# Kernel tuning notes

Hardware: AMD Instinct MI355X
Metric: run time of the kernel (lower is better)

The kernel has to match this reference:

```python
import jax, jax.numpy as jnp
import numpy as np


def setup_inputs() -> dict:
    key = jax.random.key(0)
    ks = jax.random.split(key, 8)
    B, N, C = 8, 4096, 128
    x = jax.random.normal(ks[0], (B, N, C), dtype=jnp.float32)
    spatial_pos = jax.random.randint(ks[1], (1, N, N), 0, 6, dtype=jnp.int32)
    sc = 1.0 / np.sqrt(C)
    W1 = jax.random.normal(ks[2], (C, C), dtype=jnp.float32) * sc
    b1 = jax.random.normal(ks[3], (C,), dtype=jnp.float32) * 0.01
    W2 = jax.random.normal(ks[4], (C, C // 8), dtype=jnp.float32) * sc
    b2 = jax.random.normal(ks[5], (C // 8,), dtype=jnp.float32) * 0.01
    Wb = jax.random.normal(ks[6], (C + C // 8, C), dtype=jnp.float32) * (1.0 / np.sqrt(C + C // 8))
    bb = jax.random.normal(ks[7], (C,), dtype=jnp.float32) * 0.01
    return {"x": x, "spatial_pos": spatial_pos, "W1": W1, "b1": b1,
            "W2": W2, "b2": b2, "Wb": Wb, "bb": bb}


def reference(x, spatial_pos, W1, b1, W2, b2, Wb, bb):
    # s=1, l=2: scale k=1 uses mask (spatial_pos <= 1), k=2 uses (spatial_pos == 2)
    sp = spatial_pos[0]                      # [N, N], batch-invariant
    m1 = (sp <= 1).astype(x.dtype)           # [N, N]
    m2 = (sp == 2).astype(x.dtype)           # [N, N]
    h1 = x @ W1 + b1                         # [B, N, C]
    h2 = x @ W2 + b2                         # [B, N, C//8]
    # torch.bmm(mask.expand(B,-1,-1), h) == einsum over shared mask
    f1 = jnp.einsum('ij,bjc->bic', m1, h1)   # [B, N, C]
    f2 = jnp.einsum('ij,bjc->bic', m2, h2)   # [B, N, C//8]
    feats = jnp.concatenate([f1, f2], axis=-1)  # [B, N, C + C//8]
    return feats @ Wb + bb                   # [B, N, output_dim]
```

## Files before the change

kernel.cpp:

```cpp
#include <hip/hip_runtime.h>
#include <stdint.h>

typedef unsigned short u16;
typedef __attribute__((ext_vector_type(8))) short short8;
typedef __attribute__((ext_vector_type(4))) float f32x4;
typedef __attribute__((ext_vector_type(16))) float f32x16;

#define MFMA __builtin_amdgcn_mfma_f32_16x16x32_bf16
#define MFMA32 __builtin_amdgcn_mfma_f32_32x32x16_bf16

__device__ __forceinline__ u16 f2bf(float f) {
  union { float f; uint32_t u; } v; v.f = f;
  return (u16)((v.u + 0x7FFFu + ((v.u >> 16) & 1u)) >> 16);
}

#define GLOAD16(gp, lp) \
  __builtin_amdgcn_global_load_lds((const __attribute__((address_space(1))) uint32_t*)(gp), \
                                   (__attribute__((address_space(3))) uint32_t*)(lp), 16, 0, 0)

#define WS_H    0
#define WS_Q1   9502720
#define WS_Q2   9503232
#define WS_M1P  9503744
#define WS_M2P  11600896
#define WS_RS1  13698048
#define WS_RS2  13714432
#define WS_WSB  13730816

__global__ __launch_bounds__(256) void k0(const int* __restrict__ sp,
                                          unsigned long long* __restrict__ m1p,
                                          unsigned long long* __restrict__ m2p,
                                          float* __restrict__ rs1, float* __restrict__ rs2,
                                          const float* __restrict__ W1, const float* __restrict__ Wb,
                                          const float* __restrict__ b1, const float* __restrict__ b2,
                                          const float* __restrict__ W2,
                                          float* __restrict__ q1, float* __restrict__ q2,
                                          u16* __restrict__ wsbg) {
  const int tid = threadIdx.x;
  if (blockIdx.x < 1024) {
    int wave = tid >> 6, lane = tid & 63;
    int i = blockIdx.x * 4 + wave;
    const int* rowp = sp + (size_t)i * 4096;
    int c1 = 0, c2 = 0;
    for (int w = 0; w < 64; ++w) {
      int v = rowp[w * 64 + lane];
      unsigned long long bb1 = __ballot(v <= 1);
      unsigned long long bb2 = __ballot(v == 2);
      if (lane == 0) {
        m1p[(size_t)w * 4096 + i] = bb1;
        m2p[(size_t)w * 4096 + i] = bb2;
        c1 += __popcll(bb1);
        c2 += __popcll(bb2);
      }
    }
    if (lane == 0) { rs1[i] = (float)c1; rs2[i] = (float)c2; }
    return;
  }
  int idx = (int)(blockIdx.x - 1024) * 256 + tid;
  int a = idx >> 7, c = idx & 127;
  float acc = 0.f;
  for (int k = 0; k < 128; ++k) acc += W1[a * 128 + k] * Wb[k * 128 + c];
  wsbg[(((a >> 3) * 144) + c) * 8 + (a & 7)] = f2bf(acc);
  if (idx < 2048) {
    int k = idx >> 4, nn2 = idx & 15;
    wsbg[(((k >> 3) * 144) + 128 + nn2) * 8 + (k & 7)] = f2bf(W2[k * 16 + nn2]);
  }
  if (idx < 128) {
    float s1 = 0.f, s2 = 0.f;
    for (int k = 0; k < 128; ++k) s1 += b1[k] * Wb[k * 128 + idx];
    for (int k = 0; k < 16; ++k)  s2 += b2[k] * Wb[(128 + k) * 128 + idx];
    q1[idx] = s1; q2[idx] = s2;
  }
}

__global__ __launch_bounds__(256, 2) void kproj(const float* __restrict__ x,
                                                const u16* __restrict__ wsbg,
                                                u16* __restrict__ H) {
  __shared__ u16 wsb[18432];
  __shared__ u16 xs[64 * 136];
  __shared__ u16 hs[64 * 146];
  const int tid = threadIdx.x;
  const int bid = blockIdx.x;
  const int b = bid >> 6;
  const int kt = bid & 63;
  const size_t r0 = (size_t)b * 4096 + (size_t)kt * 64;

#pragma unroll
  for (int i = 0; i < 9; ++i)
    GLOAD16(wsbg + (i * 256 + tid) * 8, (char*)&wsb[0] + (i * 256 + tid) * 16);
  {
    const float* xp = x + (r0 + (tid >> 2)) * 128 + (tid & 3) * 32;
    u16* xd = xs + (tid >> 2) * 136 + (tid & 3) * 32;
#pragma unroll
    for (int i = 0; i < 4; ++i) {
      f32x4 a = ((const f32x4*)xp)[i * 2];
      f32x4 bq = ((const f32x4*)xp)[i * 2 + 1];
      short8 pk;
      pk[0] = (short)f2bf(a[0]); pk[1] = (short)f2bf(a[1]);
      pk[2] = (short)f2bf(a[2]); pk[3] = (short)f2bf(a[3]);
      pk[4] = (short)f2bf(bq[0]); pk[5] = (short)f2bf(bq[1]);
      pk[6] = (short)f2bf(bq[2]); pk[7] = (short)f2bf(bq[3]);
      *(short8*)(xd + i * 8) = pk;
    }
  }
  __syncthreads();

  const int w = tid >> 6, l = tid & 63, lr = l & 15, lg = l >> 4;
  f32x4 acc[9];
  f32x4 zz = {0.f, 0.f, 0.f, 0.f};
#pragma unroll
  for (int fn = 0; fn < 9; ++fn) acc[fn] = zz;
#pragma unroll
  for (int kf = 0; kf < 4; ++kf) {
    short8 af = *(const short8*)(xs + (w * 16 + lr) * 136 + kf * 32 + lg * 8);
#pragma unroll
    for (int fn = 0; fn < 9; ++fn) {
      short8 bf = *(const short8*)(wsb + (((kf * 4 + lg) * 144) + fn * 16 + lr) * 8);
      acc[fn] = MFMA(af, bf, acc[fn], 0, 0, 0);
    }
  }
  __syncthreads();
#pragma unroll
  for (int fn = 0; fn < 9; ++fn)
#pragma unroll
    for (int g = 0; g < 4; ++g)
      hs[(w * 16 + lg * 4 + g) * 146 + fn * 16 + lr] = f2bf(acc[fn][g]);
  __syncthreads();
  const size_t base = (size_t)kt * 73728 + (size_t)b * 9216;
  for (int i = 0; i < 5; ++i) {
    int ch = i * 256 + tid;
    if (ch < 1152) {
      union { u16 s[8]; uint4 v; } pk;
      size_t di;
      if (ch < 1024) {
        int cb = ch >> 8, ks = (ch >> 6) & 3, ll = ch & 63;
        int row = ks * 16 + (ll >> 5) * 8;
        int col = cb * 32 + (ll & 31);
#pragma unroll
        for (int e = 0; e < 8; ++e) pk.s[e] = hs[(row + e) * 146 + col];
        di = base + (size_t)((cb * 4 + ks) * 512 + ll * 8);
      } else {
        int c2 = ch - 1024;
        int kf = c2 >> 6, ll = c2 & 63;
        int row = kf * 32 + (ll >> 4) * 8;
        int col = 128 + (ll & 15);
#pragma unroll
        for (int e = 0; e < 8; ++e) pk.s[e] = hs[(row + e) * 146 + col];
        di = base + (size_t)(8192 + kf * 512 + ll * 8);
      }
      *(uint4*)(H + di) = pk.v;
    }
  }
}

__device__ __forceinline__ short8 expand_byte(uint32_t wd, int sh) {
  uint32_t b = (wd >> sh) & 0xFFu;
  uint32_t t = b * 0x8001u;
  union { uint32_t u[4]; short8 s; } r;
  r.u[0] = (t & 0x00010001u) * 0x3F80u;
  r.u[1] = (t & 0x00040004u) * 0x0FE0u;
  r.u[2] = (t & 0x00100010u) * 0x03F8u;
  r.u[3] = (t & 0x00400040u) * 0x00FEu;
  return r.s;
}

__global__ __launch_bounds__(512, 2) void kb1(const u16* __restrict__ H,
                                              const char* __restrict__ M1b,
                                              const char* __restrict__ M2b,
                                              const float* __restrict__ rs1, const float* __restrict__ rs2,
                                              const float* __restrict__ q1, const float* __restrict__ q2,
                                              const float* __restrict__ Wb, const float* __restrict__ bb,
                                              float* __restrict__ out) {
  __shared__ u16 bt[3][9216];
  __shared__ u16 mkb[3][1024];
  __shared__ float f2pf[2][128][16];
  __shared__ u16 f2s[128 * 40];
  __shared__ u16 wb2s[2048];

  const int tid = threadIdx.x;
  const int bid = blockIdx.x;
  const int b = bid & 7;
  const int i0 = (bid >> 3) * 128;

  const int w = tid >> 6, l = tid & 63, lr = l & 15, lg = l >> 4;
  const int h2 = w >> 2, cb = w & 3;
  const int rg0 = h2 * 2, rg1 = h2 * 2 + 1;
  const int kfm = h2;
  const int rt0 = cb * 2, rt1 = cb * 2 + 1;
  const int sh32 = (l >> 5) * 8;
  const int lgsh = lg * 8;

  const u16* pB0 = H + (size_t)b * 9216 + (size_t)tid * 8;
  const u16* pB1 = H + (size_t)b * 9216 + (size_t)(512 + tid) * 8;
  const u16* pB2 = H + (size_t)b * 9216 + (size_t)(1024 + tid) * 8;
  const int mc = tid - 128;
  const char* pM = ((mc & 64) ? M2b : M1b) + (size_t)i0 * 8 + (size_t)(mc & 63) * 16;
  const int dB0 = tid * 16, dB1 = (512 + tid) * 16, dB2 = (1024 + tid) * 16;
  const int dM = ((mc >> 6) & 1) * 1024 + (mc & 63) * 16;

#define STAGE(BUF) { \
    GLOAD16(pB0, (char*)&bt[BUF][0] + dB0); \
    GLOAD16(pB1, (char*)&bt[BUF][0] + dB1); \
    if (tid < 128) GLOAD16(pB2, (char*)&bt[BUF][0] + dB2); \
    else if (tid < 256) GLOAD16(pM, (char*)&mkb[BUF][0] + dM); \
    pB0 += 73728; pB1 += 73728; pB2 += 73728; pM += 32768; }

  const int fb0 = (cb * 4) * 512 + l * 8;
  const int fm0 = 8192 + kfm * 512 + l * 8;

  f32x16 am0, am1;
  f32x4 acc2a, acc2b;
#pragma unroll
  for (int i = 0; i < 16; ++i) { am0[i] = 0.f; am1[i] = 0.f; }
  acc2a[0] = acc2a[1] = acc2a[2] = acc2a[3] = 0.f;
  acc2b[0] = acc2b[1] = acc2b[2] = acc2b[3] = 0.f;

#define WAITV { if (w < 4) asm volatile("s_waitcnt vmcnt(3)" ::: "memory"); \
                else asm volatile("s_waitcnt vmcnt(2)" ::: "memory"); }

#define COMPUTE(BUF) { \
    const u16* src_ = &bt[BUF][0]; \
    const char* mk_ = (const char*)&mkb[BUF][0]; \
    uint2 cA_ = *(const uint2*)(mk_ + (rg0 * 32 + (l & 31)) * 8); \
    uint2 cB_ = *(const uint2*)(mk_ + (rg1 * 32 + (l & 31)) * 8); \
    uint32_t cm0_ = *(const uint32_t*)(mk_ + 1024 + (rt0 * 16 + lr) * 8 + kfm * 4); \
    uint32_t cm1_ = *(const uint32_t*)(mk_ + 1024 + (rt1 * 16 + lr) * 8 + kfm * 4); \
    short8 bf0_ = *(const short8*)(src_ + fb0); \
    short8 bf1_ = *(const short8*)(src_ + fb0 + 512); \
    short8 bf2_ = *(const short8*)(src_ + fb0 + 1024); \
    short8 bf3_ = *(const short8*)(src_ + fb0 + 1536); \
    short8 bm_  = *(const short8*)(src_ + fm0); \
    short8 eA0_ = expand_byte(cA_.x, sh32); \
    short8 eA1_ = expand_byte(cA_.x, sh32 + 16); \
    short8 eA2_ = expand_byte(cA_.y, sh32); \
    short8 eA3_ = expand_byte(cA_.y, sh32 + 16); \
    short8 eB0_ = expand_byte(cB_.x, sh32); \
    short8 eB1_ = expand_byte(cB_.x, sh32 + 16); \
    short8 eB2_ = expand_byte(cB_.y, sh32); \
    short8 eB3_ = expand_byte(cB_.y, sh32 + 16); \
    short8 em0_ = expand_byte(cm0_, lgsh); \
    short8 em1_ = expand_byte(cm1_, lgsh); \
    __builtin_amdgcn_s_setprio(1); \
    am0 = MFMA32(eA0_, bf0_, am0, 0, 0, 0); \
    am1 = MFMA32(eB0_, bf0_, am1, 0, 0, 0); \
    am0 = MFMA32(eA1_, bf1_, am0, 0, 0, 0); \
    am1 = MFMA32(eB1_, bf1_, am1, 0, 0, 0); \
    am0 = MFMA32(eA2_, bf2_, am0, 0, 0, 0); \
    am1 = MFMA32(eB2_, bf2_, am1, 0, 0, 0); \
    am0 = MFMA32(eA3_, bf3_, am0, 0, 0, 0); \
    am1 = MFMA32(eB3_, bf3_, am1, 0, 0, 0); \
    acc2a = MFMA(em0_, bm_, acc2a, 0, 0, 0); \
    acc2b = MFMA(em1_, bm_, acc2b, 0, 0, 0); \
    __builtin_amdgcn_s_setprio(0); }

#define PHASE(BUF, BUF2) { WAITV; __builtin_amdgcn_s_barrier(); STAGE(BUF2); COMPUTE(BUF) }

  STAGE(0);
  STAGE(1);

#pragma unroll
  for (int i = 0; i < 4; ++i) {
    int e = i * 512 + tid;
    int cbw = e >> 9, rem = e & 511, ll = rem >> 3, ee = rem & 7;
    wb2s[e] = f2bf(Wb[(128 + (ll >> 5) * 8 + ee) * 128 + cbw * 32 + (ll & 31)]);
  }

  for (int it = 0; it < 20; ++it) {
    PHASE(0, 2);
    PHASE(1, 0);
    PHASE(2, 1);
  }
  PHASE(0, 2);
  PHASE(1, 0);
  { WAITV; __builtin_amdgcn_s_barrier(); COMPUTE(2) }
  { asm volatile("s_waitcnt vmcnt(0)" ::: "memory");
    __builtin_amdgcn_s_barrier(); COMPUTE(0) }

#pragma unroll
  for (int gg = 0; gg < 4; ++gg) {
    f2pf[kfm][rt0 * 16 + lg * 4 + gg][lr] = acc2a[gg];
    f2pf[kfm][rt1 * 16 + lg * 4 + gg][lr] = acc2b[gg];
  }
  __syncthreads();
#pragma unroll
  for (int j = 0; j < 4; ++j) {
    int e = j * 512 + tid;
    int row = e >> 4, col = e & 15;
    f2s[row * 40 + col] = f2bf(f2pf[0][row][col] + f2pf[1][row][col]);
  }
  __syncthreads();

  {
    short8 bw_ = *(const short8*)(wb2s + cb * 512 + l * 8);
    short8 afA = *(const short8*)(f2s + (rg0 * 32 + (l & 31)) * 40 + sh32);
    short8 afB = *(const short8*)(f2s + (rg1 * 32 + (l & 31)) * 40 + sh32);
    am0 = MFMA32(afA, bw_, am0, 0, 0, 0);
    am1 = MFMA32(afB, bw_, am1, 0, 0, 0);
  }

  const int colA = cb * 32 + (l & 31);
  const float q1v = q1[colA], q2v = q2[colA], bbv = bb[colA];
#pragma unroll
  for (int r = 0; r < 16; ++r) {
    int rr = (r & 3) + 8 * (r >> 2) + 4 * (l >> 5);
    {
      int row = rg0 * 32 + rr;
      float r1 = rs1[i0 + row], r2 = rs2[i0 + row];
      out[((size_t)b * 4096 + i0 + row) * 128 + colA] = am0[r] + r1 * q1v + r2 * q2v + bbv;
    }
    {
      int row = rg1 * 32 + rr;
      float r1 = rs1[i0 + row], r2 = rs2[i0 + row];
      out[((size_t)b * 4096 + i0 + row) * 128 + colA] = am1[r] + r1 * q1v + r2 * q2v + bbv;
    }
  }
}

extern "C" void kernel_launch(void* const* d_in, const int* in_sizes, int n_in,
                              void* d_out, int out_size, void* d_ws, size_t ws_size,
                              hipStream_t stream) {
  const float* x  = (const float*)d_in[0];
  const int*   sp = (const int*)d_in[1];
  const float* W1 = (const float*)d_in[2];
  const float* b1 = (const float*)d_in[3];
  const float* W2 = (const float*)d_in[4];
  const float* b2 = (const float*)d_in[5];
  const float* Wb = (const float*)d_in[6];
  const float* bb = (const float*)d_in[7];
  float* out = (float*)d_out;
  char* ws = (char*)d_ws;

  u16* H = (u16*)(ws + WS_H);
  float* q1 = (float*)(ws + WS_Q1);
  float* q2 = (float*)(ws + WS_Q2);
  unsigned long long* m1p = (unsigned long long*)(ws + WS_M1P);
  unsigned long long* m2p = (unsigned long long*)(ws + WS_M2P);
  float* rs1 = (float*)(ws + WS_RS1);
  float* rs2 = (float*)(ws + WS_RS2);
  u16* wsbg = (u16*)(ws + WS_WSB);

  k0<<<1088, 256, 0, stream>>>(sp, m1p, m2p, rs1, rs2, W1, Wb, b1, b2, W2, q1, q2, wsbg);
  kproj<<<512, 256, 0, stream>>>(x, wsbg, H);
  kb1<<<256, 512, 0, stream>>>(H, (const char*)m1p, (const char*)m2p,
                               rs1, rs2, q1, q2, Wb, bb, out);
}
```

Before: 97.00 us.

## Halve kb1 row tile to 64 rows and double grid to 512 blocks

The main mask-aggregation kernel now processes 64 output rows per block instead of 128, and the grid doubles to 512 blocks. Each wave keeps one 32x32 accumulator and one 16x16 accumulator instead of two of each, and the mask staging and wait counts are adjusted to match. The aim is more blocks across the CUs and fewer registers per wave for better occupancy. The cost is that every block still streams the full H matrix for its batch, so reads of H from global or L2 roughly double, and each loaded tile feeds half as many MFMAs.

```diff
diff --git a/kernel.cpp b/kernel.cpp
--- a/kernel.cpp
+++ b/kernel.cpp
@@ -173,20 +173,18 @@
                                               float* __restrict__ out) {
   __shared__ u16 bt[3][9216];
   __shared__ u16 mkb[3][1024];
-  __shared__ float f2pf[2][128][16];
-  __shared__ u16 f2s[128 * 40];
+  __shared__ float f2pf[2][64][16];
+  __shared__ u16 f2s[64 * 40];
   __shared__ u16 wb2s[2048];
 
   const int tid = threadIdx.x;
   const int bid = blockIdx.x;
   const int b = bid & 7;
-  const int i0 = (bid >> 3) * 128;
+  const int i0 = (bid >> 3) * 64;
 
   const int w = tid >> 6, l = tid & 63, lr = l & 15, lg = l >> 4;
-  const int h2 = w >> 2, cb = w & 3;
-  const int rg0 = h2 * 2, rg1 = h2 * 2 + 1;
-  const int kfm = h2;
-  const int rt0 = cb * 2, rt1 = cb * 2 + 1;
+  const int rg = w >> 2, cb = w & 3;
+  const int rt = w & 3, kfm = w >> 2;
   const int sh32 = (l >> 5) * 8;
   const int lgsh = lg * 8;
 
@@ -194,63 +192,50 @@
   const u16* pB1 = H + (size_t)b * 9216 + (size_t)(512 + tid) * 8;
   const u16* pB2 = H + (size_t)b * 9216 + (size_t)(1024 + tid) * 8;
   const int mc = tid - 128;
-  const char* pM = ((mc & 64) ? M2b : M1b) + (size_t)i0 * 8 + (size_t)(mc & 63) * 16;
+  const char* pM = ((mc < 32) ? M1b : M2b) + (size_t)i0 * 8 + (size_t)(mc & 31) * 16;
   const int dB0 = tid * 16, dB1 = (512 + tid) * 16, dB2 = (1024 + tid) * 16;
-  const int dM = ((mc >> 6) & 1) * 1024 + (mc & 63) * 16;
+  const int dM = mc * 16;
 
 #define STAGE(BUF) { \
     GLOAD16(pB0, (char*)&bt[BUF][0] + dB0); \
     GLOAD16(pB1, (char*)&bt[BUF][0] + dB1); \
     if (tid < 128) GLOAD16(pB2, (char*)&bt[BUF][0] + dB2); \
-    else if (tid < 256) GLOAD16(pM, (char*)&mkb[BUF][0] + dM); \
+    else if (tid < 192) GLOAD16(pM, (char*)&mkb[BUF][0] + dM); \
     pB0 += 73728; pB1 += 73728; pB2 += 73728; pM += 32768; }
 
   const int fb0 = (cb * 4) * 512 + l * 8;
   const int fm0 = 8192 + kfm * 512 + l * 8;
 
-  f32x16 am0, am1;
-  f32x4 acc2a, acc2b;
-#pragma unroll
-  for (int i = 0; i < 16; ++i) { am0[i] = 0.f; am1[i] = 0.f; }
-  acc2a[0] = acc2a[1] = acc2a[2] = acc2a[3] = 0.f;
-  acc2b[0] = acc2b[1] = acc2b[2] = acc2b[3] = 0.f;
-
-#define WAITV { if (w < 4) asm volatile("s_waitcnt vmcnt(3)" ::: "memory"); \
+  f32x16 am;
+  f32x4 acc2;
+#pragma unroll
+  for (int i = 0; i < 16; ++i) am[i] = 0.f;
+  acc2[0] = acc2[1] = acc2[2] = acc2[3] = 0.f;
+
+#define WAITV { if (w < 3) asm volatile("s_waitcnt vmcnt(3)" ::: "memory"); \
                 else asm volatile("s_waitcnt vmcnt(2)" ::: "memory"); }
 
 #define COMPUTE(BUF) { \
     const u16* src_ = &bt[BUF][0]; \
     const char* mk_ = (const char*)&mkb[BUF][0]; \
-    uint2 cA_ = *(const uint2*)(mk_ + (rg0 * 32 + (l & 31)) * 8); \
-    uint2 cB_ = *(const uint2*)(mk_ + (rg1 * 32 + (l & 31)) * 8); \
-    uint32_t cm0_ = *(const uint32_t*)(mk_ + 1024 + (rt0 * 16 + lr) * 8 + kfm * 4); \
-    uint32_t cm1_ = *(const uint32_t*)(mk_ + 1024 + (rt1 * 16 + lr) * 8 + kfm * 4); \
+    uint2 cA_ = *(const uint2*)(mk_ + (rg * 32 + (l & 31)) * 8); \
+    uint32_t cm_ = *(const uint32_t*)(mk_ + 512 + (rt * 16 + lr) * 8 + kfm * 4); \
     short8 bf0_ = *(const short8*)(src_ + fb0); \
     short8 bf1_ = *(const short8*)(src_ + fb0 + 512); \
     short8 bf2_ = *(const short8*)(src_ + fb0 + 1024); \
     short8 bf3_ = *(const short8*)(src_ + fb0 + 1536); \
     short8 bm_  = *(const short8*)(src_ + fm0); \
-    short8 eA0_ = expand_byte(cA_.x, sh32); \
-    short8 eA1_ = expand_byte(cA_.x, sh32 + 16); \
-    short8 eA2_ = expand_byte(cA_.y, sh32); \
-    short8 eA3_ = expand_byte(cA_.y, sh32 + 16); \
-    short8 eB0_ = expand_byte(cB_.x, sh32); \
-    short8 eB1_ = expand_byte(cB_.x, sh32 + 16); \
-    short8 eB2_ = expand_byte(cB_.y, sh32); \
-    short8 eB3_ = expand_byte(cB_.y, sh32 + 16); \
-    short8 em0_ = expand_byte(cm0_, lgsh); \
-    short8 em1_ = expand_byte(cm1_, lgsh); \
+    short8 e0_ = expand_byte(cA_.x, sh32); \
+    short8 e1_ = expand_byte(cA_.x, sh32 + 16); \
+    short8 e2_ = expand_byte(cA_.y, sh32); \
+    short8 e3_ = expand_byte(cA_.y, sh32 + 16); \
+    short8 em_ = expand_byte(cm_, lgsh); \
     __builtin_amdgcn_s_setprio(1); \
-    am0 = MFMA32(eA0_, bf0_, am0, 0, 0, 0); \
-    am1 = MFMA32(eB0_, bf0_, am1, 0, 0, 0); \
-    am0 = MFMA32(eA1_, bf1_, am0, 0, 0, 0); \
-    am1 = MFMA32(eB1_, bf1_, am1, 0, 0, 0); \
-    am0 = MFMA32(eA2_, bf2_, am0, 0, 0, 0); \
-    am1 = MFMA32(eB2_, bf2_, am1, 0, 0, 0); \
-    am0 = MFMA32(eA3_, bf3_, am0, 0, 0, 0); \
-    am1 = MFMA32(eB3_, bf3_, am1, 0, 0, 0); \
-    acc2a = MFMA(em0_, bm_, acc2a, 0, 0, 0); \
-    acc2b = MFMA(em1_, bm_, acc2b, 0, 0, 0); \
+    am = MFMA32(e0_, bf0_, am, 0, 0, 0); \
+    am = MFMA32(e1_, bf1_, am, 0, 0, 0); \
+    am = MFMA32(e2_, bf2_, am, 0, 0, 0); \
+    am = MFMA32(e3_, bf3_, am, 0, 0, 0); \
+    acc2 = MFMA(em_, bm_, acc2, 0, 0, 0); \
     __builtin_amdgcn_s_setprio(0); }
 
 #define PHASE(BUF, BUF2) { WAITV; __builtin_amdgcn_s_barrier(); STAGE(BUF2); COMPUTE(BUF) }
@@ -277,13 +262,11 @@
     __builtin_amdgcn_s_barrier(); COMPUTE(0) }
 
 #pragma unroll
-  for (int gg = 0; gg < 4; ++gg) {
-    f2pf[kfm][rt0 * 16 + lg * 4 + gg][lr] = acc2a[gg];
-    f2pf[kfm][rt1 * 16 + lg * 4 + gg][lr] = acc2b[gg];
-  }
-  __syncthreads();
-#pragma unroll
-  for (int j = 0; j < 4; ++j) {
+  for (int gg = 0; gg < 4; ++gg)
+    f2pf[kfm][rt * 16 + lg * 4 + gg][lr] = acc2[gg];
+  __syncthreads();
+#pragma unroll
+  for (int j = 0; j < 2; ++j) {
     int e = j * 512 + tid;
     int row = e >> 4, col = e & 15;
     f2s[row * 40 + col] = f2bf(f2pf[0][row][col] + f2pf[1][row][col]);
@@ -292,27 +275,17 @@
 
   {
     short8 bw_ = *(const short8*)(wb2s + cb * 512 + l * 8);
-    short8 afA = *(const short8*)(f2s + (rg0 * 32 + (l & 31)) * 40 + sh32);
-    short8 afB = *(const short8*)(f2s + (rg1 * 32 + (l & 31)) * 40 + sh32);
-    am0 = MFMA32(afA, bw_, am0, 0, 0, 0);
-    am1 = MFMA32(afB, bw_, am1, 0, 0, 0);
+    short8 af_ = *(const short8*)(f2s + (rg * 32 + (l & 31)) * 40 + sh32);
+    am = MFMA32(af_, bw_, am, 0, 0, 0);
   }
 
   const int colA = cb * 32 + (l & 31);
   const float q1v = q1[colA], q2v = q2[colA], bbv = bb[colA];
 #pragma unroll
   for (int r = 0; r < 16; ++r) {
-    int rr = (r & 3) + 8 * (r >> 2) + 4 * (l >> 5);
-    {
-      int row = rg0 * 32 + rr;
-      float r1 = rs1[i0 + row], r2 = rs2[i0 + row];
-      out[((size_t)b * 4096 + i0 + row) * 128 + colA] = am0[r] + r1 * q1v + r2 * q2v + bbv;
-    }
-    {
-      int row = rg1 * 32 + rr;
-      float r1 = rs1[i0 + row], r2 = rs2[i0 + row];
-      out[((size_t)b * 4096 + i0 + row) * 128 + colA] = am1[r] + r1 * q1v + r2 * q2v + bbv;
-    }
+    int row = rg * 32 + (r & 3) + 8 * (r >> 2) + 4 * (l >> 5);
+    float r1 = rs1[i0 + row], r2 = rs2[i0 + row];
+    out[((size_t)b * 4096 + i0 + row) * 128 + colA] = am[r] + r1 * q1v + r2 * q2v + bbv;
   }
 }
 
@@ -341,6 +314,6 @@
 
   k0<<<1088, 256, 0, stream>>>(sp, m1p, m2p, rs1, rs2, W1, Wb, b1, b2, W2, q1, q2, wsbg);
   kproj<<<512, 256, 0, stream>>>(x, wsbg, H);
-  kb1<<<256, 512, 0, stream>>>(H, (const char*)m1p, (const char*)m2p,
+  kb1<<<512, 512, 0, stream>>>(H, (const char*)m1p, (const char*)m2p,
                                rs1, rs2, q1, q2, Wb, bb, out);
 }
```

Result: faster. 88.46 us (-8.8%).
